# Performance work log

Measured on AMD Instinct MI355X. Metric: run time of the kernel, lower is better.

Reference implementation:

```python
import jax, jax.numpy as jnp
import numpy as np

VAR_N, LEVELS, NCELLS, PRED_N = 4, 17, 56, 12
D = VAR_N * LEVELS          # 68
FLAT = VAR_N * D            # 272 = ntiles * interm in CrossConnector
T = 4096
DT = 0.1                    # fused-ODE solver step of the LTC cell


def _var_encoder(x, w1, b1, w2, b2, w3, b3, w4, b4, w5, b5):
    # nn.Sequential(Linear, ReLU, Linear, ReLU, Linear, ReLU, Linear, ReLU, Linear)
    h = jax.nn.relu(x @ w1 + b1)
    h = jax.nn.relu(h @ w2 + b2)
    h = jax.nn.relu(h @ w3 + b3)
    h = jax.nn.relu(h @ w4 + b4)
    return h @ w5 + b5


def _run_ltc(seq, wx, wh, b, a, tau, wout, bout):
    def cell(h, u):
        f = jax.nn.sigmoid(u @ wx + h @ wh + b)           # gated synaptic activation
        return (h + DT * f * a) / (1.0 + DT * (1.0 / (tau + 0.5) + f))

    def step_obs(h, u):
        h2 = cell(h, u)
        return h2, h2 @ wout + bout

    hT, vs1 = jax.lax.scan(step_obs, jnp.zeros((NCELLS,), seq.dtype), seq)

    def step_pred(carry, _):
        h, v = carry
        h2 = cell(h, v)
        v2 = h2 @ wout + bout
        return (h2, v2), v2

    _, vs2 = jax.lax.scan(step_pred, (hT, vs1[-1]), None, length=PRED_N)
    return jnp.concatenate([vs1, vs2], axis=0)        # (T+PRED_N, LEVELS)


def setup_inputs() -> dict:
    key = jax.random.key(0)
    ks = iter(jax.random.split(key, 64))
    d = {"x": jax.random.normal(next(ks), (T, D), jnp.float32)}

    def add_ve(prefix, inp, out):
        dims = [(inp, inp), (inp, inp), (inp, out), (out, out), (out, out)]
        for i, (fi, fo) in enumerate(dims, 1):
            d[f"{prefix}w{i}"] = jax.random.normal(next(ks), (fi, fo), jnp.float32) / np.sqrt(fi)
            d[f"{prefix}b{i}"] = jax.random.normal(next(ks), (fo,), jnp.float32) * 0.01

    add_ve("p", D, D)          # preproc  VarEncoder(68,68)
    add_ve("c1", LEVELS, D)    # CrossConnector inner VarEncoder(17,68)
    add_ve("c2", FLAT, D)      # CrossConnector outer VarEncoder(272,68)

    d["ltc_wx"] = jax.random.normal(next(ks), (VAR_N, LEVELS, NCELLS), jnp.float32) / np.sqrt(LEVELS)
    d["ltc_wh"] = jax.random.normal(next(ks), (VAR_N, NCELLS, NCELLS), jnp.float32) / np.sqrt(NCELLS)
    d["ltc_b"] = jax.random.normal(next(ks), (VAR_N, NCELLS), jnp.float32) * 0.01
    d["ltc_a"] = jax.random.normal(next(ks), (VAR_N, NCELLS), jnp.float32)
    d["ltc_tau"] = jax.random.uniform(next(ks), (VAR_N, NCELLS), jnp.float32)
    d["ltc_wout"] = jax.random.normal(next(ks), (VAR_N, NCELLS, LEVELS), jnp.float32) / np.sqrt(NCELLS)
    d["ltc_bout"] = jax.random.normal(next(ks), (VAR_N, LEVELS), jnp.float32) * 0.01
    return d


def reference(x, pw1, pb1, pw2, pb2, pw3, pb3, pw4, pb4, pw5, pb5,
              c1w1, c1b1, c1w2, c1b2, c1w3, c1b3, c1w4, c1b4, c1w5, c1b5,
              c2w1, c2b1, c2w2, c2b2, c2w3, c2b3, c2w4, c2b4, c2w5, c2b5,
              ltc_wx, ltc_wh, ltc_b, ltc_a, ltc_tau, ltc_wout, ltc_bout):
    pre = _var_encoder(x, pw1, pb1, pw2, pb2, pw3, pb3, pw4, pb4, pw5, pb5)   # (T, 68)
    xs = pre.reshape(VAR_N, -1, LEVELS)                                       # (4, T, 17) row-major, as torch.reshape
    vs = jax.vmap(_run_ltc)(xs, ltc_wx, ltc_wh, ltc_b, ltc_a, ltc_tau,
                            ltc_wout, ltc_bout)                               # (4, T+12, 17)
    vs = jnp.transpose(vs, (1, 0, 2))                                         # (T+12, 4, 17)
    y = jax.nn.relu(_var_encoder(vs, c1w1, c1b1, c1w2, c1b2, c1w3, c1b3,
                                 c1w4, c1b4, c1w5, c1b5))                     # (T+12, 4, 68)
    y = y.reshape(y.shape[0], -1)                                             # (T+12, 272)
    return _var_encoder(y, c2w1, c2b1, c2w2, c2b2, c2w3, c2b3,
                        c2w4, c2b4, c2w5, c2b5)                               # (T+12, 68)
```

## Files before the change

kernel.cpp:

```cpp
#include <hip/hip_runtime.h>
#include <hip/hip_bf16.h>
#include <math.h>

#define VAR_N 4
#define LEVELS 17
#define NCELLS 56
#define PRED_N 12
#define TSTEPS 4096
#define TROWS (TSTEPS + PRED_N)
#define DT 0.1f
#define RPB 8
#define LOG2E 1.44269504088896340736f
#define TB 16

static __device__ __forceinline__ float rl(float x, int lane) {
    return __int_as_float(__builtin_amdgcn_readlane(__float_as_int(x), lane));
}
static __device__ __forceinline__ float rcpf(float x) {
    return __builtin_amdgcn_rcpf(x);
}

__global__ void pre_g_kernel(const float* __restrict__ x,
                             const float* __restrict__ w1, const float* __restrict__ b1,
                             const float* __restrict__ w2, const float* __restrict__ b2,
                             const float* __restrict__ w3, const float* __restrict__ b3,
                             const float* __restrict__ w4, const float* __restrict__ b4,
                             const float* __restrict__ w5, const float* __restrict__ b5,
                             const float* __restrict__ wx, const float* __restrict__ bvec,
                             float* __restrict__ g) {
    __shared__ float lds[2 * RPB * 68];
    float* bufA = lds;
    float* bufB = lds + RPB * 68;
    const int r0 = blockIdx.x * RPB;
    const int tid = threadIdx.x;

    for (int idx = tid; idx < RPB * 68; idx += 256)
        bufA[idx] = x[(size_t)r0 * 68 + idx];
    __syncthreads();

    const float* Ws[5] = {w1, w2, w3, w4, w5};
    const float* Bs[5] = {b1, b2, b3, b4, b5};
    for (int L = 0; L < 5; ++L) {
        const float* __restrict__ W = Ws[L];
        const bool act = (L < 4);
        if (tid < 68) {
            const int j = tid;
            float acc[RPB];
            float bj = Bs[L][j];
#pragma unroll
            for (int r = 0; r < RPB; ++r) acc[r] = bj;
            for (int k = 0; k + 4 <= 68; k += 4) {
                float w0v = W[(k + 0) * 68 + j];
                float w1v = W[(k + 1) * 68 + j];
                float w2v = W[(k + 2) * 68 + j];
                float w3v = W[(k + 3) * 68 + j];
#pragma unroll
                for (int r = 0; r < RPB; ++r) {
                    const float4 hx = *(const float4*)(bufA + r * 68 + k);
                    acc[r] = fmaf(hx.x, w0v, fmaf(hx.y, w1v,
                              fmaf(hx.z, w2v, fmaf(hx.w, w3v, acc[r]))));
                }
            }
#pragma unroll
            for (int r = 0; r < RPB; ++r)
                bufB[r * 68 + j] = act ? fmaxf(acc[r], 0.f) : acc[r];
        }
        __syncthreads();
        float* t = bufA; bufA = bufB; bufB = t;
    }

    for (int idx = tid; idx < RPB * 4 * NCELLS; idx += 256) {
        int r = idx / 224;
        int rem = idx - r * 224;
        int q = rem / NCELLS;
        int j = rem - q * NCELLS;
        int gr = r0 + r;
        int v = gr >> 10;
        int trow = ((gr & 1023) << 2) + q;
        const float* arow = bufA + r * 68 + q * LEVELS;
        float acc = bvec[v * NCELLS + j];
#pragma unroll
        for (int l = 0; l < LEVELS; ++l)
            acc = fmaf(arow[l], wx[(v * LEVELS + l) * NCELLS + j], acc);
        g[((size_t)(v * NCELLS + j)) * TSTEPS + trow] = acc * LOG2E;
    }
}

__global__ void __launch_bounds__(64, 1) scan_kernel(
    const float* __restrict__ g, const float* __restrict__ wh,
    const float* __restrict__ a, const float* __restrict__ tau,
    const float* __restrict__ wx, const float* __restrict__ wout,
    const float* __restrict__ bout, const float* __restrict__ b,
    float* __restrict__ H) {
    typedef float v2 __attribute__((ext_vector_type(2)));
    const int v = blockIdx.x;
    const int lane = threadIdx.x;
    const bool active = lane < NCELLS;
    const int j = active ? lane : (NCELLS - 1);
    __shared__ __align__(16) float hbuf[64];

    v2 whp[28];
#pragma unroll
    for (int q = 0; q < 28; ++q) {
        float w0 = active ? wh[((size_t)v * NCELLS + 2 * q + 0) * NCELLS + lane] * LOG2E : 0.f;
        float w1 = active ? wh[((size_t)v * NCELLS + 2 * q + 1) * NCELLS + lane] * LOG2E : 0.f;
        v2 t; t.x = w0; t.y = w1;
        whp[q] = t;
    }
    const float alpha = active ? DT * a[v * NCELLS + lane] : 0.f;
    const float cden = active ? 1.f + DT / (tau[v * NCELLS + lane] + 0.5f) : 1.f;

    const float4* __restrict__ gv4 = (const float4*)(g + ((size_t)v * NCELLS + j) * TSTEPS);
    float* __restrict__ hp = H + (size_t)v * TROWS * NCELLS + lane;

    auto cell = [&](float h, float gcur) -> float {
        hbuf[lane] = h;
        const float4* h4 = (const float4*)hbuf;
        float4 hv[14];
#pragma unroll
        for (int q = 0; q < 14; ++q) hv[q] = h4[q];
        v2 a0 = {0.f, 0.f}, a1 = {0.f, 0.f}, a2 = {0.f, 0.f}, a3 = {0.f, 0.f};
#pragma unroll
        for (int q = 0; q < 7; ++q) {
            float4 hq0 = hv[2 * q];
            float4 hq1 = hv[2 * q + 1];
            v2 p0; p0.x = hq0.x; p0.y = hq0.y;
            v2 p1; p1.x = hq0.z; p1.y = hq0.w;
            v2 p2; p2.x = hq1.x; p2.y = hq1.y;
            v2 p3; p3.x = hq1.z; p3.y = hq1.w;
            a0 = __builtin_elementwise_fma(p0, whp[4 * q + 0], a0);
            a1 = __builtin_elementwise_fma(p1, whp[4 * q + 1], a1);
            a2 = __builtin_elementwise_fma(p2, whp[4 * q + 2], a2);
            a3 = __builtin_elementwise_fma(p3, whp[4 * q + 3], a3);
        }
        v2 s = (a0 + a1) + (a2 + a3);
        float z2 = (gcur + s.x) + s.y;
        float zc = fmaxf(z2, -80.f);
        float e = __builtin_amdgcn_exp2f(-zc);
        float t1 = 1.f + e;
        float num = fmaf(h, t1, alpha);
        float den = fmaf(cden, t1, DT);
        float hn = num * rcpf(den);
        __builtin_amdgcn_sched_group_barrier(0x200, 1, 0);
        __builtin_amdgcn_sched_group_barrier(0x100, 14, 0);
        __builtin_amdgcn_sched_group_barrier(0x002, 40, 0);
        return hn;
    };

    float h = 0.f;
    float4 gq = gv4[0];
    for (int tq = 0; tq < TSTEPS / 4; ++tq) {
        float4 gn = gq;
        if (tq + 1 < TSTEPS / 4) gn = gv4[tq + 1];
        h = cell(h, gq.x); if (active) hp[0 * NCELLS] = h;
        h = cell(h, gq.y); if (active) hp[1 * NCELLS] = h;
        h = cell(h, gq.z); if (active) hp[2 * NCELLS] = h;
        h = cell(h, gq.w); if (active) hp[3 * NCELLS] = h;
        hp += 4 * NCELLS;
        gq = gn;
    }

    float wxcol[LEVELS];
#pragma unroll
    for (int l = 0; l < LEVELS; ++l)
        wxcol[l] = active ? wx[(v * LEVELS + l) * NCELLS + lane] * LOG2E : 0.f;
    float wtc[NCELLS];
#pragma unroll
    for (int jj = 0; jj < NCELLS; ++jj)
        wtc[jj] = (lane < LEVELS) ? wout[((size_t)v * NCELLS + jj) * LEVELS + lane] : 0.f;
    const float bj = active ? b[v * NCELLS + lane] * LOG2E : 0.f;
    const float boutl = (lane < LEVELS) ? bout[v * LEVELS + lane] : 0.f;

    float vv = boutl;
#pragma unroll
    for (int jj = 0; jj < NCELLS; ++jj) vv = fmaf(rl(h, jj), wtc[jj], vv);

    for (int i = 0; i < PRED_N; ++i) {
        float z2 = bj;
#pragma unroll
        for (int l = 0; l < LEVELS; ++l) z2 = fmaf(rl(vv, l), wxcol[l], z2);
#pragma unroll
        for (int k = 0; k < NCELLS; ++k) {
            float wk = (k & 1) ? whp[k >> 1].y : whp[k >> 1].x;
            z2 = fmaf(rl(h, k), wk, z2);
        }
        float zc = fmaxf(z2, -80.f);
        float e = __builtin_amdgcn_exp2f(-zc);
        float t1 = 1.f + e;
        h = fmaf(h, t1, alpha) * rcpf(fmaf(cden, t1, DT));
        if (active) hp[0] = h;
        hp += NCELLS;
        vv = boutl;
#pragma unroll
        for (int jj = 0; jj < NCELLS; ++jj) vv = fmaf(rl(h, jj), wtc[jj], vv);
    }
}

__global__ void __launch_bounds__(320) c1c2_kernel(
    const float* __restrict__ H,
    const float* __restrict__ wout, const float* __restrict__ bout,
    const float* __restrict__ c1w1, const float* __restrict__ c1b1,
    const float* __restrict__ c1w2, const float* __restrict__ c1b2,
    const float* __restrict__ c1w3, const float* __restrict__ c1b3,
    const float* __restrict__ c1w4, const float* __restrict__ c1b4,
    const float* __restrict__ c1w5, const float* __restrict__ c1b5,
    const float* __restrict__ c2w1, const float* __restrict__ c2b1,
    const float* __restrict__ c2w2, const float* __restrict__ c2b2,
    const float* __restrict__ c2w3, const float* __restrict__ c2b3,
    const float* __restrict__ c2w4, const float* __restrict__ c2b4,
    const float* __restrict__ c2w5, const float* __restrict__ c2b5,
    float* __restrict__ out) {
    __shared__ __align__(16) float sH[64 * 56];
    __shared__ __align__(16) float sW1[4 * 17 * 56];
    __shared__ float sB1[4 * 17];
    __shared__ __align__(16) float bA[64 * 20];
    __shared__ __align__(16) float bB[64 * 20];
    __shared__ __align__(16) float bY[TB * 272];
    __shared__ __align__(16) float bZ[TB * 272];
    const int t0 = blockIdx.x * TB;
    const int tid = threadIdx.x;

    for (int idx = tid; idx < 4 * 17 * 56; idx += 320) {
        int v = idx / (17 * 56);
        int rem = idx - v * (17 * 56);
        int l = rem / 56, k = rem - (rem / 56) * 56;
        float acc = 0.f;
#pragma unroll
        for (int m = 0; m < 17; ++m)
            acc = fmaf(wout[(v * 56 + k) * 17 + m], c1w1[m * 17 + l], acc);
        sW1[idx] = acc;
    }
    for (int idx = tid; idx < 68; idx += 320) {
        int v = idx / 17, l = idx - (idx / 17) * 17;
        float acc = c1b1[l];
#pragma unroll
        for (int m = 0; m < 17; ++m)
            acc = fmaf(bout[v * 17 + m], c1w1[m * 17 + l], acc);
        sB1[idx] = acc;
    }
    for (int idx = tid; idx < 64 * 56; idx += 320) {
        int row = idx / 56, j = idx - (idx / 56) * 56;
        int rt = row >> 2, v = row & 3;
        int t = t0 + rt;
        sH[idx] = (t < TROWS) ? H[((size_t)v * TROWS + t) * 56 + j] : 0.f;
    }
    __syncthreads();

    if (tid < 272) {
        int l = tid % 17, s = tid / 17;
        int v = s & 3, q = s >> 2;
        const float* Wrow = sW1 + (v * 17 + l) * 56;
        float bl = sB1[v * 17 + l];
        float acc[4];
#pragma unroll
        for (int r = 0; r < 4; ++r) acc[r] = bl;
        for (int k = 0; k < 56; k += 4) {
            float4 w = *(const float4*)(Wrow + k);
#pragma unroll
            for (int r = 0; r < 4; ++r) {
                const float4 hx = *(const float4*)(sH + ((4 * q + r) * 4 + v) * 56 + k);
                acc[r] = fmaf(hx.x, w.x, fmaf(hx.y, w.y,
                          fmaf(hx.z, w.z, fmaf(hx.w, w.w, acc[r]))));
            }
        }
#pragma unroll
        for (int r = 0; r < 4; ++r)
            bA[((4 * q + r) * 4 + v) * 20 + l] = fmaxf(acc[r], 0.f);
    }
    __syncthreads();

    if (tid < 272) {
        int l = tid % 17, s = tid / 17;
        float acc[4];
        float bl = c1b2[l];
#pragma unroll
        for (int r = 0; r < 4; ++r) acc[r] = bl;
        for (int k = 0; k + 4 <= 17; k += 4) {
            float w0 = c1w2[(k + 0) * 17 + l], w1 = c1w2[(k + 1) * 17 + l];
            float w2 = c1w2[(k + 2) * 17 + l], w3 = c1w2[(k + 3) * 17 + l];
#pragma unroll
            for (int r = 0; r < 4; ++r) {
                const float4 hx = *(const float4*)(bA + (4 * s + r) * 20 + k);
                acc[r] = fmaf(hx.x, w0, fmaf(hx.y, w1, fmaf(hx.z, w2, fmaf(hx.w, w3, acc[r]))));
            }
        }
        float w16 = c1w2[16 * 17 + l];
#pragma unroll
        for (int r = 0; r < 4; ++r) {
            acc[r] = fmaf(bA[(4 * s + r) * 20 + 16], w16, acc[r]);
            bB[(4 * s + r) * 20 + l] = fmaxf(acc[r], 0.f);
        }
    }
    __syncthreads();

    if (tid < 272) {
        int j = tid % 68, gr = tid / 68;
        float acc[16];
        float bj = c1b3[j];
#pragma unroll
        for (int r = 0; r < 16; ++r) acc[r] = bj;
        for (int k = 0; k + 4 <= 17; k += 4) {
            float w0 = c1w3[(k + 0) * 68 + j], w1 = c1w3[(k + 1) * 68 + j];
            float w2 = c1w3[(k + 2) * 68 + j], w3 = c1w3[(k + 3) * 68 + j];
#pragma unroll
            for (int r = 0; r < 16; ++r) {
                const float4 hx = *(const float4*)(bB + (16 * gr + r) * 20 + k);
                acc[r] = fmaf(hx.x, w0, fmaf(hx.y, w1, fmaf(hx.z, w2, fmaf(hx.w, w3, acc[r]))));
            }
        }
        float w16 = c1w3[16 * 68 + j];
#pragma unroll
        for (int r = 0; r < 16; ++r) {
            acc[r] = fmaf(bB[(16 * gr + r) * 20 + 16], w16, acc[r]);
            bY[(16 * gr + r) * 68 + j] = fmaxf(acc[r], 0.f);
        }
    }
    __syncthreads();

#pragma unroll
    for (int LL = 0; LL < 2; ++LL) {
        const float* W = LL ? c1w5 : c1w4;
        const float* B = LL ? c1b5 : c1b4;
        const float* inb = LL ? bZ : bY;
        float* outb = LL ? bY : bZ;
        if (tid < 272) {
            int j = tid % 68, gr = tid / 68;
            float acc[16];
            float bj = B[j];
#pragma unroll
            for (int r = 0; r < 16; ++r) acc[r] = bj;
            for (int k = 0; k < 68; k += 4) {
                float w0 = W[(k + 0) * 68 + j], w1 = W[(k + 1) * 68 + j];
                float w2 = W[(k + 2) * 68 + j], w3 = W[(k + 3) * 68 + j];
#pragma unroll
                for (int r = 0; r < 16; ++r) {
                    const float4 hx = *(const float4*)(inb + (16 * gr + r) * 68 + k);
                    acc[r] = fmaf(hx.x, w0, fmaf(hx.y, w1, fmaf(hx.z, w2, fmaf(hx.w, w3, acc[r]))));
                }
            }
#pragma unroll
            for (int r = 0; r < 16; ++r)
                outb[(16 * gr + r) * 68 + j] = fmaxf(acc[r], 0.f);
        }
        __syncthreads();
    }

#pragma unroll
    for (int LL = 0; LL < 2; ++LL) {
        const float* W = LL ? c2w2 : c2w1;
        const float* B = LL ? c2b2 : c2b1;
        const float* inb = LL ? bZ : bY;
        float* outb = LL ? bY : bZ;
        if (tid < 272) {
            int j = tid;
            float acc[16];
            float bj = B[j];
#pragma unroll
            for (int r = 0; r < 16; ++r) acc[r] = bj;
            for (int k = 0; k < 272; k += 4) {
                float w0 = W[(size_t)(k + 0) * 272 + j], w1 = W[(size_t)(k + 1) * 272 + j];
                float w2 = W[(size_t)(k + 2) * 272 + j], w3 = W[(size_t)(k + 3) * 272 + j];
#pragma unroll
                for (int r = 0; r < 16; ++r) {
                    const float4 hx = *(const float4*)(inb + r * 272 + k);
                    acc[r] = fmaf(hx.x, w0, fmaf(hx.y, w1, fmaf(hx.z, w2, fmaf(hx.w, w3, acc[r]))));
                }
            }
#pragma unroll
            for (int r = 0; r < 16; ++r)
                outb[r * 272 + j] = fmaxf(acc[r], 0.f);
        }
        __syncthreads();
    }

    if (tid < 272) {
        int j = tid % 68, gr = tid / 68;
        float acc[4];
        float bj = c2b3[j];
#pragma unroll
        for (int r = 0; r < 4; ++r) acc[r] = bj;
        for (int k = 0; k < 272; k += 4) {
            float w0 = c2w3[(size_t)(k + 0) * 68 + j], w1 = c2w3[(size_t)(k + 1) * 68 + j];
            float w2 = c2w3[(size_t)(k + 2) * 68 + j], w3 = c2w3[(size_t)(k + 3) * 68 + j];
#pragma unroll
            for (int r = 0; r < 4; ++r) {
                const float4 hx = *(const float4*)(bY + (4 * gr + r) * 272 + k);
                acc[r] = fmaf(hx.x, w0, fmaf(hx.y, w1, fmaf(hx.z, w2, fmaf(hx.w, w3, acc[r]))));
            }
        }
#pragma unroll
        for (int r = 0; r < 4; ++r)
            bZ[(4 * gr + r) * 68 + j] = fmaxf(acc[r], 0.f);
    }
    __syncthreads();

    if (tid < 272) {
        int j = tid % 68, gr = tid / 68;
        float acc[4];
        float bj = c2b4[j];
#pragma unroll
        for (int r = 0; r < 4; ++r) acc[r] = bj;
        for (int k = 0; k < 68; k += 4) {
            float w0 = c2w4[(k + 0) * 68 + j], w1 = c2w4[(k + 1) * 68 + j];
            float w2 = c2w4[(k + 2) * 68 + j], w3 = c2w4[(k + 3) * 68 + j];
#pragma unroll
            for (int r = 0; r < 4; ++r) {
                const float4 hx = *(const float4*)(bZ + (4 * gr + r) * 68 + k);
                acc[r] = fmaf(hx.x, w0, fmaf(hx.y, w1, fmaf(hx.z, w2, fmaf(hx.w, w3, acc[r]))));
            }
        }
#pragma unroll
        for (int r = 0; r < 4; ++r)
            bY[(4 * gr + r) * 68 + j] = fmaxf(acc[r], 0.f);
    }
    __syncthreads();

    if (tid < 272) {
        int j = tid % 68, gr = tid / 68;
        float acc[4];
        float bj = c2b5[j];
#pragma unroll
        for (int r = 0; r < 4; ++r) acc[r] = bj;
        for (int k = 0; k < 68; k += 4) {
            float w0 = c2w5[(k + 0) * 68 + j], w1 = c2w5[(k + 1) * 68 + j];
            float w2 = c2w5[(k + 2) * 68 + j], w3 = c2w5[(k + 3) * 68 + j];
#pragma unroll
            for (int r = 0; r < 4; ++r) {
                const float4 hx = *(const float4*)(bY + (4 * gr + r) * 68 + k);
                acc[r] = fmaf(hx.x, w0, fmaf(hx.y, w1, fmaf(hx.z, w2, fmaf(hx.w, w3, acc[r]))));
            }
        }
#pragma unroll
        for (int r = 0; r < 4; ++r)
            bZ[(4 * gr + r) * 68 + j] = acc[r];
    }
    __syncthreads();

    for (int idx = tid; idx < TB * 68; idx += 320) {
        int r = idx / 68, c = idx - (idx / 68) * 68;
        int t = t0 + r;
        if (t < TROWS) out[(size_t)t * 68 + c] = bZ[r * 68 + c];
    }
}

extern "C" void kernel_launch(void* const* d_in, const int* in_sizes, int n_in,
                              void* d_out, int out_size, void* d_ws, size_t ws_size,
                              hipStream_t stream) {
    const float* x = (const float*)d_in[0];
    const float* pw[5] = {(const float*)d_in[1], (const float*)d_in[3], (const float*)d_in[5],
                          (const float*)d_in[7], (const float*)d_in[9]};
    const float* pb[5] = {(const float*)d_in[2], (const float*)d_in[4], (const float*)d_in[6],
                          (const float*)d_in[8], (const float*)d_in[10]};
    const float* c1w[5] = {(const float*)d_in[11], (const float*)d_in[13], (const float*)d_in[15],
                           (const float*)d_in[17], (const float*)d_in[19]};
    const float* c1b[5] = {(const float*)d_in[12], (const float*)d_in[14], (const float*)d_in[16],
                           (const float*)d_in[18], (const float*)d_in[20]};
    const float* c2w[5] = {(const float*)d_in[21], (const float*)d_in[23], (const float*)d_in[25],
                           (const float*)d_in[27], (const float*)d_in[29]};
    const float* c2b[5] = {(const float*)d_in[22], (const float*)d_in[24], (const float*)d_in[26],
                           (const float*)d_in[28], (const float*)d_in[30]};
    const float* ltc_wx = (const float*)d_in[31];
    const float* ltc_wh = (const float*)d_in[32];
    const float* ltc_b = (const float*)d_in[33];
    const float* ltc_a = (const float*)d_in[34];
    const float* ltc_tau = (const float*)d_in[35];
    const float* ltc_wout = (const float*)d_in[36];
    const float* ltc_bout = (const float*)d_in[37];

    float* ws = (float*)d_ws;
    float* g = ws;
    float* H = g + 917504;
    float* out = (float*)d_out;

    pre_g_kernel<<<TSTEPS / RPB, 256, 0, stream>>>(
        x, pw[0], pb[0], pw[1], pb[1], pw[2], pb[2], pw[3], pb[3], pw[4], pb[4],
        ltc_wx, ltc_b, g);

    scan_kernel<<<VAR_N, 64, 0, stream>>>(g, ltc_wh, ltc_a, ltc_tau, ltc_wx,
                                          ltc_wout, ltc_bout, ltc_b, H);

    c1c2_kernel<<<(TROWS + TB - 1) / TB, 320, 0, stream>>>(
        H, ltc_wout, ltc_bout,
        c1w[0], c1b[0], c1w[1], c1b[1], c1w[2], c1b[2], c1w[3], c1b[3], c1w[4], c1b[4],
        c2w[0], c2b[0], c2w[1], c2b[1], c2w[2], c2b[2], c2w[3], c2b[3], c2w[4], c2b[4],
        out);
}
```

Measured before the change: 1.107 ms.

## Halve c1c2 row tile, drop per-block fused wout·c1w1 precompute, widen c2 layers

Shrinks the c1c2 kernel's time tile from 16 to 8 rows and the block from 320 to 256 threads, doubling the grid. It stops rebuilding the fused wout×c1w1 weight matrix in LDS in every block and instead applies the LTC output projection as its own layer. That adds one more 17-wide layer and barrier. The 272-wide c2 layers now compute two output columns per thread using float2 weight loads, and the c2 tail layers are folded into a loop. The intent is to remove redundant per-block weight setup and improve occupancy, at the cost of more blocks that each reload the weights and more idle threads (136 of 256 active).

```diff
diff --git a/kernel.cpp b/kernel.cpp
--- a/kernel.cpp
+++ b/kernel.cpp
@@ -11,7 +11,7 @@
 #define DT 0.1f
 #define RPB 8
 #define LOG2E 1.44269504088896340736f
-#define TB 16
+#define TB 8
 
 static __device__ __forceinline__ float rl(float x, int lane) {
     return __int_as_float(__builtin_amdgcn_readlane(__float_as_int(x), lane));
@@ -196,7 +196,7 @@
     }
 }
 
-__global__ void __launch_bounds__(320) c1c2_kernel(
+__global__ void __launch_bounds__(256) c1c2_kernel(
     const float* __restrict__ H,
     const float* __restrict__ wout, const float* __restrict__ bout,
     const float* __restrict__ c1w1, const float* __restrict__ c1b1,
@@ -210,91 +210,79 @@
     const float* __restrict__ c2w4, const float* __restrict__ c2b4,
     const float* __restrict__ c2w5, const float* __restrict__ c2b5,
     float* __restrict__ out) {
-    __shared__ __align__(16) float sH[64 * 56];
-    __shared__ __align__(16) float sW1[4 * 17 * 56];
-    __shared__ float sB1[4 * 17];
-    __shared__ __align__(16) float bA[64 * 20];
-    __shared__ __align__(16) float bB[64 * 20];
+    __shared__ __align__(16) float sH[32 * 56];
+    __shared__ __align__(16) float nA[32 * 20];
+    __shared__ __align__(16) float nB[32 * 20];
     __shared__ __align__(16) float bY[TB * 272];
     __shared__ __align__(16) float bZ[TB * 272];
     const int t0 = blockIdx.x * TB;
     const int tid = threadIdx.x;
 
-    for (int idx = tid; idx < 4 * 17 * 56; idx += 320) {
-        int v = idx / (17 * 56);
-        int rem = idx - v * (17 * 56);
-        int l = rem / 56, k = rem - (rem / 56) * 56;
-        float acc = 0.f;
-#pragma unroll
-        for (int m = 0; m < 17; ++m)
-            acc = fmaf(wout[(v * 56 + k) * 17 + m], c1w1[m * 17 + l], acc);
-        sW1[idx] = acc;
-    }
-    for (int idx = tid; idx < 68; idx += 320) {
-        int v = idx / 17, l = idx - (idx / 17) * 17;
-        float acc = c1b1[l];
-#pragma unroll
-        for (int m = 0; m < 17; ++m)
-            acc = fmaf(bout[v * 17 + m], c1w1[m * 17 + l], acc);
-        sB1[idx] = acc;
-    }
-    for (int idx = tid; idx < 64 * 56; idx += 320) {
-        int row = idx / 56, j = idx - (idx / 56) * 56;
-        int rt = row >> 2, v = row & 3;
-        int t = t0 + rt;
-        sH[idx] = (t < TROWS) ? H[((size_t)v * TROWS + t) * 56 + j] : 0.f;
+    for (int idx = tid; idx < 32 * 56; idx += 256) {
+        int row = idx / 56, jj = idx - (idx / 56) * 56;
+        int tq = row >> 2, v = row & 3;
+        int t = t0 + tq;
+        sH[idx] = (t < TROWS) ? H[((size_t)v * TROWS + t) * 56 + jj] : 0.f;
     }
     __syncthreads();
 
-    if (tid < 272) {
-        int l = tid % 17, s = tid / 17;
-        int v = s & 3, q = s >> 2;
-        const float* Wrow = sW1 + (v * 17 + l) * 56;
-        float bl = sB1[v * 17 + l];
+    if (tid < 136) {
+        int l = tid % 17;
+        int rg = tid / 17;
+        int v = rg & 3, th = rg >> 2;
         float acc[4];
-#pragma unroll
-        for (int r = 0; r < 4; ++r) acc[r] = bl;
+        float bl = bout[v * 17 + l];
+#pragma unroll
+        for (int q = 0; q < 4; ++q) acc[q] = bl;
         for (int k = 0; k < 56; k += 4) {
-            float4 w = *(const float4*)(Wrow + k);
-#pragma unroll
-            for (int r = 0; r < 4; ++r) {
-                const float4 hx = *(const float4*)(sH + ((4 * q + r) * 4 + v) * 56 + k);
-                acc[r] = fmaf(hx.x, w.x, fmaf(hx.y, w.y,
-                          fmaf(hx.z, w.z, fmaf(hx.w, w.w, acc[r]))));
-            }
-        }
-#pragma unroll
-        for (int r = 0; r < 4; ++r)
-            bA[((4 * q + r) * 4 + v) * 20 + l] = fmaxf(acc[r], 0.f);
+            float w0 = wout[(v * 56 + k + 0) * 17 + l];
+            float w1 = wout[(v * 56 + k + 1) * 17 + l];
+            float w2 = wout[(v * 56 + k + 2) * 17 + l];
+            float w3 = wout[(v * 56 + k + 3) * 17 + l];
+#pragma unroll
+            for (int q = 0; q < 4; ++q) {
+                const float4 hx = *(const float4*)(sH + ((th * 4 + q) * 4 + v) * 56 + k);
+                acc[q] = fmaf(hx.x, w0, fmaf(hx.y, w1, fmaf(hx.z, w2, fmaf(hx.w, w3, acc[q]))));
+            }
+        }
+#pragma unroll
+        for (int q = 0; q < 4; ++q) nA[((th * 4 + q) * 4 + v) * 20 + l] = acc[q];
     }
     __syncthreads();
 
-    if (tid < 272) {
-        int l = tid % 17, s = tid / 17;
-        float acc[4];
-        float bl = c1b2[l];
-#pragma unroll
-        for (int r = 0; r < 4; ++r) acc[r] = bl;
-        for (int k = 0; k + 4 <= 17; k += 4) {
-            float w0 = c1w2[(k + 0) * 17 + l], w1 = c1w2[(k + 1) * 17 + l];
-            float w2 = c1w2[(k + 2) * 17 + l], w3 = c1w2[(k + 3) * 17 + l];
-#pragma unroll
-            for (int r = 0; r < 4; ++r) {
-                const float4 hx = *(const float4*)(bA + (4 * s + r) * 20 + k);
-                acc[r] = fmaf(hx.x, w0, fmaf(hx.y, w1, fmaf(hx.z, w2, fmaf(hx.w, w3, acc[r]))));
-            }
-        }
-        float w16 = c1w2[16 * 17 + l];
-#pragma unroll
-        for (int r = 0; r < 4; ++r) {
-            acc[r] = fmaf(bA[(4 * s + r) * 20 + 16], w16, acc[r]);
-            bB[(4 * s + r) * 20 + l] = fmaxf(acc[r], 0.f);
-        }
-    }
-    __syncthreads();
-
-    if (tid < 272) {
-        int j = tid % 68, gr = tid / 68;
+#pragma unroll
+    for (int LL = 0; LL < 2; ++LL) {
+        const float* W = LL ? c1w2 : c1w1;
+        const float* B = LL ? c1b2 : c1b1;
+        const float* in = LL ? nB : nA;
+        float* ob = LL ? nA : nB;
+        if (tid < 136) {
+            int l = tid % 17;
+            int rg = tid / 17;
+            float acc[4];
+            float bl = B[l];
+#pragma unroll
+            for (int q = 0; q < 4; ++q) acc[q] = bl;
+            for (int k = 0; k + 4 <= 17; k += 4) {
+                float w0 = W[(k + 0) * 17 + l], w1 = W[(k + 1) * 17 + l];
+                float w2 = W[(k + 2) * 17 + l], w3 = W[(k + 3) * 17 + l];
+#pragma unroll
+                for (int q = 0; q < 4; ++q) {
+                    const float4 hx = *(const float4*)(in + (rg * 4 + q) * 20 + k);
+                    acc[q] = fmaf(hx.x, w0, fmaf(hx.y, w1, fmaf(hx.z, w2, fmaf(hx.w, w3, acc[q]))));
+                }
+            }
+            float w16 = W[16 * 17 + l];
+#pragma unroll
+            for (int q = 0; q < 4; ++q)
+                ob[(rg * 4 + q) * 20 + l] = fmaxf(fmaf(in[(rg * 4 + q) * 20 + 16], w16, acc[q]), 0.f);
+        }
+        __syncthreads();
+    }
+
+    if (tid < 136) {
+        int j = tid % 68;
+        int rg = tid / 68;
         float acc[16];
         float bj = c1b3[j];
 #pragma unroll
@@ -304,16 +292,14 @@
             float w2 = c1w3[(k + 2) * 68 + j], w3 = c1w3[(k + 3) * 68 + j];
 #pragma unroll
             for (int r = 0; r < 16; ++r) {
-                const float4 hx = *(const float4*)(bB + (16 * gr + r) * 20 + k);
+                const float4 hx = *(const float4*)(nA + (rg * 16 + r) * 20 + k);
                 acc[r] = fmaf(hx.x, w0, fmaf(hx.y, w1, fmaf(hx.z, w2, fmaf(hx.w, w3, acc[r]))));
             }
         }
         float w16 = c1w3[16 * 68 + j];
 #pragma unroll
-        for (int r = 0; r < 16; ++r) {
-            acc[r] = fmaf(bB[(16 * gr + r) * 20 + 16], w16, acc[r]);
-            bY[(16 * gr + r) * 68 + j] = fmaxf(acc[r], 0.f);
-        }
+        for (int r = 0; r < 16; ++r)
+            bY[(rg * 16 + r) * 68 + j] = fmaxf(fmaf(nA[(rg * 16 + r) * 20 + 16], w16, acc[r]), 0.f);
     }
     __syncthreads();
 
@@ -321,10 +307,11 @@
     for (int LL = 0; LL < 2; ++LL) {
         const float* W = LL ? c1w5 : c1w4;
         const float* B = LL ? c1b5 : c1b4;
-        const float* inb = LL ? bZ : bY;
-        float* outb = LL ? bY : bZ;
-        if (tid < 272) {
-            int j = tid % 68, gr = tid / 68;
+        const float* in = LL ? bZ : bY;
+        float* ob = LL ? bY : bZ;
+        if (tid < 136) {
+            int j = tid % 68;
+            int rg = tid / 68;
             float acc[16];
             float bj = B[j];
 #pragma unroll
@@ -334,13 +321,13 @@
                 float w2 = W[(k + 2) * 68 + j], w3 = W[(k + 3) * 68 + j];
 #pragma unroll
                 for (int r = 0; r < 16; ++r) {
-                    const float4 hx = *(const float4*)(inb + (16 * gr + r) * 68 + k);
+                    const float4 hx = *(const float4*)(in + (rg * 16 + r) * 68 + k);
                     acc[r] = fmaf(hx.x, w0, fmaf(hx.y, w1, fmaf(hx.z, w2, fmaf(hx.w, w3, acc[r]))));
                 }
             }
 #pragma unroll
             for (int r = 0; r < 16; ++r)
-                outb[(16 * gr + r) * 68 + j] = fmaxf(acc[r], 0.f);
+                ob[(rg * 16 + r) * 68 + j] = fmaxf(acc[r], 0.f);
         }
         __syncthreads();
     }
@@ -349,32 +336,38 @@
     for (int LL = 0; LL < 2; ++LL) {
         const float* W = LL ? c2w2 : c2w1;
         const float* B = LL ? c2b2 : c2b1;
-        const float* inb = LL ? bZ : bY;
-        float* outb = LL ? bY : bZ;
-        if (tid < 272) {
-            int j = tid;
-            float acc[16];
-            float bj = B[j];
-#pragma unroll
-            for (int r = 0; r < 16; ++r) acc[r] = bj;
+        const float* in = LL ? bZ : bY;
+        float* ob = LL ? bY : bZ;
+        if (tid < 136) {
+            int j = 2 * tid;
+            float acc0[TB], acc1[TB];
+            float b0 = B[j], b1 = B[j + 1];
+#pragma unroll
+            for (int r = 0; r < TB; ++r) { acc0[r] = b0; acc1[r] = b1; }
             for (int k = 0; k < 272; k += 4) {
-                float w0 = W[(size_t)(k + 0) * 272 + j], w1 = W[(size_t)(k + 1) * 272 + j];
-                float w2 = W[(size_t)(k + 2) * 272 + j], w3 = W[(size_t)(k + 3) * 272 + j];
-#pragma unroll
-                for (int r = 0; r < 16; ++r) {
-                    const float4 hx = *(const float4*)(inb + r * 272 + k);
-                    acc[r] = fmaf(hx.x, w0, fmaf(hx.y, w1, fmaf(hx.z, w2, fmaf(hx.w, w3, acc[r]))));
+                float2 w0 = *(const float2*)(W + (size_t)(k + 0) * 272 + j);
+                float2 w1 = *(const float2*)(W + (size_t)(k + 1) * 272 + j);
+                float2 w2 = *(const float2*)(W + (size_t)(k + 2) * 272 + j);
+                float2 w3 = *(const float2*)(W + (size_t)(k + 3) * 272 + j);
+#pragma unroll
+                for (int r = 0; r < TB; ++r) {
+                    const float4 hx = *(const float4*)(in + r * 272 + k);
+                    acc0[r] = fmaf(hx.x, w0.x, fmaf(hx.y, w1.x, fmaf(hx.z, w2.x, fmaf(hx.w, w3.x, acc0[r]))));
+                    acc1[r] = fmaf(hx.x, w0.y, fmaf(hx.y, w1.y, fmaf(hx.z, w2.y, fmaf(hx.w, w3.y, acc1[r]))));
                 }
             }
 #pragma unroll
-            for (int r = 0; r < 16; ++r)
-                outb[r * 272 + j] = fmaxf(acc[r], 0.f);
+            for (int r = 0; r < TB; ++r) {
+                ob[r * 272 + j] = fmaxf(acc0[r], 0.f);
+                ob[r * 272 + j + 1] = fmaxf(acc1[r], 0.f);
+            }
         }
         __syncthreads();
     }
 
-    if (tid < 272) {
-        int j = tid % 68, gr = tid / 68;
+    if (tid < 136) {
+        int j = tid % 68;
+        int rg = tid / 68;
         float acc[4];
         float bj = c2b3[j];
 #pragma unroll
@@ -384,59 +377,47 @@
             float w2 = c2w3[(size_t)(k + 2) * 68 + j], w3 = c2w3[(size_t)(k + 3) * 68 + j];
 #pragma unroll
             for (int r = 0; r < 4; ++r) {
-                const float4 hx = *(const float4*)(bY + (4 * gr + r) * 272 + k);
+                const float4 hx = *(const float4*)(bY + (rg * 4 + r) * 272 + k);
                 acc[r] = fmaf(hx.x, w0, fmaf(hx.y, w1, fmaf(hx.z, w2, fmaf(hx.w, w3, acc[r]))));
             }
         }
 #pragma unroll
         for (int r = 0; r < 4; ++r)
-            bZ[(4 * gr + r) * 68 + j] = fmaxf(acc[r], 0.f);
+            bZ[(rg * 4 + r) * 68 + j] = fmaxf(acc[r], 0.f);
     }
     __syncthreads();
 
-    if (tid < 272) {
-        int j = tid % 68, gr = tid / 68;
-        float acc[4];
-        float bj = c2b4[j];
-#pragma unroll
-        for (int r = 0; r < 4; ++r) acc[r] = bj;
-        for (int k = 0; k < 68; k += 4) {
-            float w0 = c2w4[(k + 0) * 68 + j], w1 = c2w4[(k + 1) * 68 + j];
-            float w2 = c2w4[(k + 2) * 68 + j], w3 = c2w4[(k + 3) * 68 + j];
-#pragma unroll
-            for (int r = 0; r < 4; ++r) {
-                const float4 hx = *(const float4*)(bZ + (4 * gr + r) * 68 + k);
-                acc[r] = fmaf(hx.x, w0, fmaf(hx.y, w1, fmaf(hx.z, w2, fmaf(hx.w, w3, acc[r]))));
-            }
-        }
-#pragma unroll
-        for (int r = 0; r < 4; ++r)
-            bY[(4 * gr + r) * 68 + j] = fmaxf(acc[r], 0.f);
-    }
-    __syncthreads();
-
-    if (tid < 272) {
-        int j = tid % 68, gr = tid / 68;
-        float acc[4];
-        float bj = c2b5[j];
-#pragma unroll
-        for (int r = 0; r < 4; ++r) acc[r] = bj;
-        for (int k = 0; k < 68; k += 4) {
-            float w0 = c2w5[(k + 0) * 68 + j], w1 = c2w5[(k + 1) * 68 + j];
-            float w2 = c2w5[(k + 2) * 68 + j], w3 = c2w5[(k + 3) * 68 + j];
-#pragma unroll
-            for (int r = 0; r < 4; ++r) {
-                const float4 hx = *(const float4*)(bY + (4 * gr + r) * 68 + k);
-                acc[r] = fmaf(hx.x, w0, fmaf(hx.y, w1, fmaf(hx.z, w2, fmaf(hx.w, w3, acc[r]))));
-            }
-        }
-#pragma unroll
-        for (int r = 0; r < 4; ++r)
-            bZ[(4 * gr + r) * 68 + j] = acc[r];
-    }
-    __syncthreads();
-
-    for (int idx = tid; idx < TB * 68; idx += 320) {
+#pragma unroll
+    for (int LL = 0; LL < 2; ++LL) {
+        const float* W = LL ? c2w5 : c2w4;
+        const float* B = LL ? c2b5 : c2b4;
+        const float* in = LL ? bY : bZ;
+        float* ob = LL ? bZ : bY;
+        const bool act = (LL == 0);
+        if (tid < 136) {
+            int j = tid % 68;
+            int rg = tid / 68;
+            float acc[4];
+            float bj = B[j];
+#pragma unroll
+            for (int r = 0; r < 4; ++r) acc[r] = bj;
+            for (int k = 0; k < 68; k += 4) {
+                float w0 = W[(k + 0) * 68 + j], w1 = W[(k + 1) * 68 + j];
+                float w2 = W[(k + 2) * 68 + j], w3 = W[(k + 3) * 68 + j];
+#pragma unroll
+                for (int r = 0; r < 4; ++r) {
+                    const float4 hx = *(const float4*)(in + (rg * 4 + r) * 68 + k);
+                    acc[r] = fmaf(hx.x, w0, fmaf(hx.y, w1, fmaf(hx.z, w2, fmaf(hx.w, w3, acc[r]))));
+                }
+            }
+#pragma unroll
+            for (int r = 0; r < 4; ++r)
+                ob[(rg * 4 + r) * 68 + j] = act ? fmaxf(acc[r], 0.f) : acc[r];
+        }
+        __syncthreads();
+    }
+
+    for (int idx = tid; idx < TB * 68; idx += 256) {
         int r = idx / 68, c = idx - (idx / 68) * 68;
         int t = t0 + r;
         if (t < TROWS) out[(size_t)t * 68 + c] = bZ[r * 68 + c];
@@ -479,7 +460,7 @@
     scan_kernel<<<VAR_N, 64, 0, stream>>>(g, ltc_wh, ltc_a, ltc_tau, ltc_wx,
                                           ltc_wout, ltc_bout, ltc_b, H);
 
-    c1c2_kernel<<<(TROWS + TB - 1) / TB, 320, 0, stream>>>(
+    c1c2_kernel<<<(TROWS + TB - 1) / TB, 256, 0, stream>>>(
         H, ltc_wout, ltc_bout,
         c1w[0], c1b[0], c1w[1], c1b[1], c1w[2], c1b[2], c1w[3], c1b[3], c1w[4], c1b[4],
         c2w[0], c2b[0], c2w[1], c2b[1], c2w[2], c2b[2], c2w[3], c2b[3], c2w[4], c2b[4],
```

After: 1.047 ms, median of 2. 1.06x faster.
